# Performance work log

Hardware: AMD Instinct MI355X
Metric: run time of the kernel (lower is better)

Reference implementation:

```python
import jax, jax.numpy as jnp
import numpy as np

D_MODEL = 1024
N_HEADS = 16
D_K = D_MODEL // N_HEADS
THETA = 10000.0
B, S = 4, 2048


def _rope(x, positions):
    # x: [B, H, S, D_K]; positions: [S] int
    half = D_K // 2
    inv_freq = THETA ** (-jnp.arange(0, half, dtype=jnp.float32) * 2.0 / D_K)  # [half]
    ang = positions.astype(jnp.float32)[:, None] * inv_freq[None, :]  # [S, half]
    cos = jnp.cos(ang)[None, None, :, :]
    sin = jnp.sin(ang)[None, None, :, :]
    x_even = x[..., 0::2]
    x_odd = x[..., 1::2]
    out_even = x_even * cos - x_odd * sin
    out_odd = x_even * sin + x_odd * cos
    # interleave back to original layout
    out = jnp.stack([out_even, out_odd], axis=-1).reshape(x.shape)
    return out


def setup_inputs() -> dict:
    key = jax.random.key(0)
    ks = jax.random.split(key, 5)
    scale = 1.0 / np.sqrt(D_MODEL)
    return {
        "x": jax.random.normal(ks[0], (B, S, D_MODEL), dtype=jnp.float32),
        "token_positions": jnp.arange(S, dtype=jnp.int64 if jax.config.jax_enable_x64 else jnp.int32),
        "Wq": jax.random.normal(ks[1], (D_MODEL, D_MODEL), dtype=jnp.float32) * scale,
        "Wk": jax.random.normal(ks[2], (D_MODEL, D_MODEL), dtype=jnp.float32) * scale,
        "Wv": jax.random.normal(ks[3], (D_MODEL, D_MODEL), dtype=jnp.float32) * scale,
        "Wo": jax.random.normal(ks[4], (D_MODEL, D_MODEL), dtype=jnp.float32) * scale,
    }


def reference(x, token_positions, Wq, Wk, Wv, Wo):
    bsz, seq_len, _ = x.shape
    # projections (Linear_Transform: y = x @ W^T, no bias)
    def proj(W):
        h = jnp.einsum("bsd,ed->bse", x, W)
        return h.reshape(bsz, seq_len, N_HEADS, D_K).transpose(0, 2, 1, 3)  # [B,H,S,Dk]
    Q = proj(Wq)
    K = proj(Wk)
    V = proj(Wv)
    Q = _rope(Q, token_positions)
    K = _rope(K, token_positions)
    # scaled dot product attention with causal mask
    scores = jnp.einsum("bhqd,bhkd->bhqk", Q, K) / jnp.sqrt(jnp.float32(D_K))
    causal = jnp.tril(jnp.ones((seq_len, seq_len), dtype=bool))  # [S,S]
    scores = jnp.where(causal[None, None, :, :], scores, -jnp.inf)
    attn = jax.nn.softmax(scores, axis=-1)
    out = jnp.einsum("bhqk,bhkd->bhqd", attn, V)
    out = out.transpose(0, 2, 1, 3).reshape(bsz, seq_len, D_MODEL)
    return jnp.einsum("bsd,ed->bse", out, Wo)
```

## Files before the change

### kernel.cpp

```cpp
#include <hip/hip_runtime.h>
#include <hip/hip_bf16.h>
#include <cstdint>
#include <cstddef>

typedef __attribute__((ext_vector_type(4))) float f32x4;
typedef __attribute__((ext_vector_type(16))) float f32x16;
typedef __attribute__((ext_vector_type(8))) short bf16x8;
typedef unsigned int u32;
typedef unsigned short u16;


__device__ __forceinline__ u16 f2bf(float x) {
  u32 u = __builtin_bit_cast(u32, x);
  u += 0x7fffu + ((u >> 16) & 1u);
  return (u16)(u >> 16);
}

__device__ __forceinline__ u32 cvt_pk_bf16(float lo, float hi) {
  u32 r;
  asm("v_cvt_pk_bf16_f32 %0, %1, %2" : "=v"(r) : "v"(lo), "v"(hi));
  return r;
}

__device__ __forceinline__ void perm_swap(u32& a, u32& b) {
  asm("v_permlane32_swap_b32 %0, %1" : "+v"(a), "+v"(b));
}

__device__ __forceinline__ void gl_lds16(const void* g, void* l) {
  __builtin_amdgcn_global_load_lds(
      (const __attribute__((address_space(1))) u32*)(uintptr_t)g,
      (__attribute__((address_space(3))) u32*)(u32)(uintptr_t)l,
      16, 0, 0);
}

#define MFMA16(a, b, c) __builtin_amdgcn_mfma_f32_16x16x32_bf16((a), (b), (c), 0, 0, 0)
#define MFMA32(a, b, c) __builtin_amdgcn_mfma_f32_32x32x16_bf16((a), (b), (c), 0, 0, 0)


__global__ void cast_all_k(const float* __restrict__ x, const float* __restrict__ wq,
                           const float* __restrict__ wk, const float* __restrict__ wv,
                           const float* __restrict__ wo, u16* __restrict__ xb,
                           u16* __restrict__ wqb, u16* __restrict__ wkb,
                           u16* __restrict__ wvb, u16* __restrict__ wob) {
  int blk = blockIdx.x;
  const float* s; u16* d; int i;
  if (blk < 8192)       { s = x;  d = xb;  i = blk * 256; }
  else if (blk < 9216)  { s = wq; d = wqb; i = (blk - 8192) * 256; }
  else if (blk < 10240) { s = wk; d = wkb; i = (blk - 9216) * 256; }
  else if (blk < 11264) { s = wv; d = wvb; i = (blk - 10240) * 256; }
  else                  { s = wo; d = wob; i = (blk - 11264) * 256; }
  i += threadIdx.x;
  const float4 v = reinterpret_cast<const float4*>(s)[i];
  uint2 o;
  o.x = cvt_pk_bf16(v.x, v.y);
  o.y = cvt_pk_bf16(v.z, v.w);
  reinterpret_cast<uint2*>(d)[i] = o;
}


__global__ void rope_table_k(const int* __restrict__ pos, float2* __restrict__ cs) {
  int idx = blockIdx.x * 256 + threadIdx.x;
  int s = idx >> 5, i = idx & 31;
  float inv = powf(10000.0f, -(float)i * (1.0f / 32.0f));
  float ang = (float)pos[s] * inv;
  cs[idx] = float2{cosf(ang), sinf(ang)};
}


__global__ __launch_bounds__(256, 2)
void gemm_qkv(const u16* __restrict__ A, const u16* __restrict__ B,
              const float2* __restrict__ cs, u16* __restrict__ Qr,
              u16* __restrict__ Kr, u16* __restrict__ Vt, float qscale) {
  const int K = 1024;
  __shared__ u16 a_lds[2][128 * 32];
  __shared__ u16 b_lds[2][128 * 32];
  const int tid = threadIdx.x;
  const int l = tid & 63;
  const int w = tid >> 6;
  const int wm = w >> 1, wn = w & 1;
  const int bm = blockIdx.y, bn = blockIdx.x;

  const u16* Ab = A + (size_t)bm * 128 * K;
  const u16* Bb = B + (size_t)bn * 128 * K;

  auto stage = [&](int bq, int k0) {
#pragma unroll
    for (int half = 0; half < 2; ++half) {
      int t = half * 256 + tid;
      int row = t >> 2, slot = t & 3;
      int sp = slot ^ ((row >> 1) & 3);
      gl_lds16(Ab + (size_t)row * K + k0 + sp * 8, &a_lds[bq][t * 8]);
      gl_lds16(Bb + (size_t)row * K + k0 + sp * 8, &b_lds[bq][t * 8]);
    }
  };

  const f32x4 fz = {0.f, 0.f, 0.f, 0.f};
  f32x4 acc[4][4];
#pragma unroll
  for (int mi = 0; mi < 4; ++mi)
#pragma unroll
    for (int ni = 0; ni < 4; ++ni) acc[mi][ni] = fz;

  const int nk = K >> 5;
  stage(0, 0);
  int buf = 0;
  for (int kt = 0; kt < nk; ++kt) {
    __syncthreads();
    if (kt + 1 < nk) stage(buf ^ 1, (kt + 1) * 32);
    bf16x8 af[4], bf[4];
#pragma unroll
    for (int mi = 0; mi < 4; ++mi) {
      int row = wm * 64 + mi * 16 + (l & 15);
      int sp = (l >> 4) ^ ((row >> 1) & 3);
      af[mi] = *(const bf16x8*)&a_lds[buf][row * 32 + sp * 8];
    }
#pragma unroll
    for (int ni = 0; ni < 4; ++ni) {
      int row = wn * 64 + ni * 16 + (l & 15);
      int sp = (l >> 4) ^ ((row >> 1) & 3);
      bf[ni] = *(const bf16x8*)&b_lds[buf][row * 32 + sp * 8];
    }
#pragma unroll
    for (int mi = 0; mi < 4; ++mi)
#pragma unroll
      for (int ni = 0; ni < 4; ++ni)
        acc[mi][ni] = MFMA16(af[mi], bf[ni], acc[mi][ni]);
    buf ^= 1;
  }

  const int sector = bn >> 3;
  const int colb = ((bn & 7) << 7) + wn * 64;
  const int c = l & 15, h4 = l >> 4;

  if (sector == 2) {
#pragma unroll
    for (int mi = 0; mi < 4; ++mi) {
      int row = bm * 128 + wm * 64 + mi * 16 + 4 * h4;
      int b_ = row >> 11, s = row & 2047;
#pragma unroll
      for (int ni = 0; ni < 4; ++ni) {
        int cv = colb + ni * 16 + c;
        int hh = cv >> 6, dk = cv & 63;
        f32x4 v = acc[mi][ni];
        uint2 st;
        st.x = cvt_pk_bf16(v[0], v[1]);
        st.y = cvt_pk_bf16(v[2], v[3]);
        *(uint2*)&Vt[(((size_t)b_ * 16 + hh) << 17) + ((size_t)dk << 11) + s] = st;
      }
    }
  } else {
    u16* dst = sector ? Kr : Qr;
    const float scale = sector ? 1.0f : qscale;
#pragma unroll
    for (int mi = 0; mi < 4; ++mi) {
      int row0 = bm * 128 + wm * 64 + mi * 16 + 4 * h4;
#pragma unroll
      for (int ni = 0; ni < 4; ++ni) {
        int cv = colb + ni * 16 + c;
        int hh = cv >> 6, i2 = cv & 63;
        f32x4 v = acc[mi][ni];
        f32x4 pv;
#pragma unroll
        for (int j = 0; j < 4; ++j) pv[j] = __shfl_xor(v[j], 1);
        if (!(l & 1)) {
#pragma unroll
          for (int j = 0; j < 4; ++j) {
            int r = row0 + j, s = r & 2047, b_ = r >> 11;
            float2 t = cs[(s << 5) + (i2 >> 1)];
            float oe = (v[j] * t.x - pv[j] * t.y) * scale;
            float oo = (v[j] * t.y + pv[j] * t.x) * scale;
            *(u32*)&dst[(((size_t)(b_ * 16 + hh) * 2048 + s) << 6) + i2] =
                cvt_pk_bf16(oe, oo);
          }
        }
      }
    }
  }
}


__global__ __launch_bounds__(256, 2)
void gemm_bt(const u16* __restrict__ A, const u16* __restrict__ B,
             float* __restrict__ C, int M, int N, int K) {
  __shared__ u16 a_lds[2][128 * 32];
  __shared__ u16 b_lds[2][128 * 32];
  const int tid = threadIdx.x;
  const int l = tid & 63;
  const int w = tid >> 6;
  const int wm = w >> 1, wn = w & 1;
  const int bm = blockIdx.y, bn = blockIdx.x;

  const u16* Ab = A + (size_t)bm * 128 * K;
  const u16* Bb = B + (size_t)bn * 128 * K;

  auto stage = [&](int bq, int k0) {
#pragma unroll
    for (int half = 0; half < 2; ++half) {
      int t = half * 256 + tid;
      int row = t >> 2, slot = t & 3;
      int sp = slot ^ ((row >> 1) & 3);
      gl_lds16(Ab + (size_t)row * K + k0 + sp * 8, &a_lds[bq][t * 8]);
      gl_lds16(Bb + (size_t)row * K + k0 + sp * 8, &b_lds[bq][t * 8]);
    }
  };

  const f32x4 fz = {0.f, 0.f, 0.f, 0.f};
  f32x4 acc[4][4];
#pragma unroll
  for (int mi = 0; mi < 4; ++mi)
#pragma unroll
    for (int ni = 0; ni < 4; ++ni) acc[mi][ni] = fz;

  const int nk = K >> 5;
  stage(0, 0);
  int buf = 0;
  for (int kt = 0; kt < nk; ++kt) {
    __syncthreads();
    if (kt + 1 < nk) stage(buf ^ 1, (kt + 1) * 32);
    bf16x8 af[4], bf[4];
#pragma unroll
    for (int mi = 0; mi < 4; ++mi) {
      int row = wm * 64 + mi * 16 + (l & 15);
      int sp = (l >> 4) ^ ((row >> 1) & 3);
      af[mi] = *(const bf16x8*)&a_lds[buf][row * 32 + sp * 8];
    }
#pragma unroll
    for (int ni = 0; ni < 4; ++ni) {
      int row = wn * 64 + ni * 16 + (l & 15);
      int sp = (l >> 4) ^ ((row >> 1) & 3);
      bf[ni] = *(const bf16x8*)&b_lds[buf][row * 32 + sp * 8];
    }
#pragma unroll
    for (int mi = 0; mi < 4; ++mi)
#pragma unroll
      for (int ni = 0; ni < 4; ++ni)
        acc[mi][ni] = MFMA16(af[mi], bf[ni], acc[mi][ni]);
    buf ^= 1;
  }

#pragma unroll
  for (int mi = 0; mi < 4; ++mi) {
    int rbase = bm * 128 + wm * 64 + mi * 16 + ((l >> 4) << 2);
#pragma unroll
    for (int ni = 0; ni < 4; ++ni) {
      int col = bn * 128 + wn * 64 + ni * 16 + (l & 15);
      f32x4 v = acc[mi][ni];
#pragma unroll
      for (int j = 0; j < 4; ++j)
        C[(size_t)(rbase + j) * N + col] = v[j];
    }
  }
}


__global__ __launch_bounds__(256, 2)
void attn_k(const u16* __restrict__ Q, const u16* __restrict__ K,
            const u16* __restrict__ V, u16* __restrict__ O) {
  const int S = 2048;
  __shared__ u16 k_lds[2][64 * 64];
  __shared__ u16 v_lds[2][64 * 64];

  const int tid = threadIdx.x, l = tid & 63, w = tid >> 6;
  const int lane31 = l & 31, hi = l >> 5;

  const int wg = blockIdx.x;
  const int idx = (wg & 7) * 64 + (wg >> 3);
  const int bh = idx >> 3, pairI = idx & 7;

  const u16* Kb = K + (size_t)bh * S * 64;
  const u16* Vb = V + (size_t)bh * 64 * S;
  const int b = bh >> 4, hd = bh & 15;

  auto stageKV = [&](int bq, int kv0) {
#pragma unroll
    for (int half = 0; half < 2; ++half) {
      int t = half * 256 + tid;
      int row = t >> 3, slot = t & 7;
      int sp = slot ^ (row & 7);
      gl_lds16(Kb + (size_t)(kv0 + row) * 64 + sp * 8, &k_lds[bq][t * 8]);
      gl_lds16(Vb + (size_t)row * S + kv0 + sp * 8, &v_lds[bq][t * 8]);
    }
  };

#pragma unroll 1
  for (int ph = 0; ph < 2; ++ph) {
    const int qi = ph ? (15 - pairI) : pairI;
    const int q0 = qi * 128;
    const int nkv = 2 * qi + 2;
    const int qrow = q0 + w * 32 + lane31;
    const u16* Qp = Q + ((size_t)bh * S + qrow) * 64;

    bf16x8 qf[4];
#pragma unroll
    for (int ks = 0; ks < 4; ++ks)
      qf[ks] = *(const bf16x8*)(Qp + ks * 16 + hi * 8);
    __builtin_amdgcn_sched_barrier(0);
    stageKV(0, 0);

    f32x16 oacc[2];
#pragma unroll
    for (int dt = 0; dt < 2; ++dt)
#pragma unroll
      for (int r = 0; r < 16; ++r) oacc[dt][r] = 0.f;
    float m_run = -1e30f, l_run = 0.f;

    int buf = 0;
#pragma unroll 1
    for (int t = 0; t < nkv; ++t) {
      if (t + 1 < nkv) {
        stageKV(buf ^ 1, (t + 1) * 64);
        __builtin_amdgcn_sched_barrier(0);
        asm volatile("s_waitcnt vmcnt(4)" ::: "memory");
      } else {
        asm volatile("s_waitcnt vmcnt(0)" ::: "memory");
      }
      __builtin_amdgcn_sched_barrier(0);
      __builtin_amdgcn_s_barrier();
      __builtin_amdgcn_sched_barrier(0);

      f32x16 sc[2];
#pragma unroll
      for (int dt = 0; dt < 2; ++dt)
#pragma unroll
        for (int r = 0; r < 16; ++r) sc[dt][r] = 0.f;
      __builtin_amdgcn_s_setprio(1);
#pragma unroll
      for (int ks = 0; ks < 4; ++ks) {
        int sp = (2 * ks + hi) ^ (lane31 & 7);
#pragma unroll
        for (int dt = 0; dt < 2; ++dt) {
          bf16x8 kf = *(const bf16x8*)&k_lds[buf][(dt * 32 + lane31) * 64 + sp * 8];
          sc[dt] = MFMA32(kf, qf[ks], sc[dt]);
        }
      }
      __builtin_amdgcn_s_setprio(0);

      bf16x8 vf[2][4];
#pragma unroll
      for (int ks = 0; ks < 4; ++ks) {
        int sp = (2 * ks + hi) ^ (lane31 & 7);
#pragma unroll
        for (int dt = 0; dt < 2; ++dt)
          vf[dt][ks] = *(const bf16x8*)&v_lds[buf][(dt * 32 + lane31) * 64 + sp * 8];
      }

      if (t >= nkv - 2) {
#pragma unroll
        for (int dt = 0; dt < 2; ++dt)
#pragma unroll
          for (int r = 0; r < 16; ++r) {
            int kvg = t * 64 + dt * 32 + (r & 3) + 8 * (r >> 2) + 4 * hi;
            if (kvg > qrow) sc[dt][r] = -1e30f;
          }
      }

      float mx = -1e30f;
#pragma unroll
      for (int dt = 0; dt < 2; ++dt)
#pragma unroll
        for (int r = 0; r < 16; ++r) mx = fmaxf(mx, sc[dt][r]);
      mx = fmaxf(mx, __shfl_xor(mx, 32));

      const bool nores = __all(mx <= m_run);
      float mnew = nores ? m_run : fmaxf(m_run, mx);
      float ps = 0.f;
#pragma unroll
      for (int dt = 0; dt < 2; ++dt)
#pragma unroll
        for (int r = 0; r < 16; ++r) {
          float e = exp2f(sc[dt][r] - mnew);
          sc[dt][r] = e;
          ps += e;
        }
      ps += __shfl_xor(ps, 32);
      if (nores) {
        l_run += ps;
      } else {
        float alpha = exp2f(m_run - mnew);
        l_run = l_run * alpha + ps;
        m_run = mnew;
#pragma unroll
        for (int dt = 0; dt < 2; ++dt)
#pragma unroll
          for (int r = 0; r < 16; ++r) oacc[dt][r] *= alpha;
      }

      union { u32 u[4]; bf16x8 v; } pf[4];
#pragma unroll
      for (int ks = 0; ks < 4; ++ks) {
        const int sidx = ks >> 1, rb = (ks & 1) * 8;
        u32 c01 = cvt_pk_bf16(sc[sidx][rb + 0], sc[sidx][rb + 1]);
        u32 c23 = cvt_pk_bf16(sc[sidx][rb + 2], sc[sidx][rb + 3]);
        u32 c45 = cvt_pk_bf16(sc[sidx][rb + 4], sc[sidx][rb + 5]);
        u32 c67 = cvt_pk_bf16(sc[sidx][rb + 6], sc[sidx][rb + 7]);
        perm_swap(c01, c45);
        perm_swap(c23, c67);
        pf[ks].u[0] = c01; pf[ks].u[1] = c23; pf[ks].u[2] = c45; pf[ks].u[3] = c67;
      }

      __builtin_amdgcn_s_setprio(1);
#pragma unroll
      for (int dt = 0; dt < 2; ++dt)
#pragma unroll
        for (int ks = 0; ks < 4; ++ks)
          oacc[dt] = MFMA32(vf[dt][ks], pf[ks].v, oacc[dt]);
      __builtin_amdgcn_s_setprio(0);

      __builtin_amdgcn_sched_barrier(0);
      __builtin_amdgcn_s_barrier();
      __builtin_amdgcn_sched_barrier(0);
      buf ^= 1;
    }

    float inv = 1.f / l_run;
    u16* Ob = O + (((size_t)(b * 2048 + qrow)) << 10) + hd * 64;
#pragma unroll
    for (int dt = 0; dt < 2; ++dt)
#pragma unroll
      for (int g = 0; g < 4; ++g) {
        uint2 st;
        st.x = cvt_pk_bf16(oacc[dt][4 * g + 0] * inv, oacc[dt][4 * g + 1] * inv);
        st.y = cvt_pk_bf16(oacc[dt][4 * g + 2] * inv, oacc[dt][4 * g + 3] * inv);
        *(uint2*)&Ob[dt * 32 + g * 8 + hi * 4] = st;
      }
  }
}


extern "C" void kernel_launch(void* const* d_in, const int* in_sizes, int n_in,
                              void* d_out, int out_size, void* d_ws, size_t ws_size,
                              hipStream_t stream) {
  (void)in_sizes; (void)n_in; (void)out_size; (void)ws_size;
  const float* x  = (const float*)d_in[0];
  const int* pos  = (const int*)d_in[1];
  const float* Wq = (const float*)d_in[2];
  const float* Wk = (const float*)d_in[3];
  const float* Wv = (const float*)d_in[4];
  const float* Wo = (const float*)d_in[5];
  float* out = (float*)d_out;

  const int S = 2048, D = 1024;
  const size_t M = (size_t)4 * S;

  char* ws = (char*)d_ws;
  size_t off = 0;
  auto alloc = [&](size_t bytes) {
    void* p = ws + off;
    off += (bytes + 255) & ~(size_t)255;
    return p;
  };
  u16* xb   = (u16*)alloc(M * D * 2);
  u16* wqb  = (u16*)alloc((size_t)D * D * 2);
  u16* wkb  = (u16*)alloc((size_t)D * D * 2);
  u16* wvb  = (u16*)alloc((size_t)D * D * 2);
  u16* wob  = (u16*)alloc((size_t)D * D * 2);
  u16* Qr   = (u16*)alloc(M * D * 2);
  u16* Kr   = (u16*)alloc(M * D * 2);
  u16* Vt   = (u16*)alloc(M * D * 2);
  u16* Ob   = (u16*)alloc(M * D * 2);
  float2* csT = (float2*)alloc((size_t)S * 32 * 8);

  cast_all_k<<<12288, 256, 0, stream>>>(x, Wq, Wk, Wv, Wo, xb, wqb, wkb, wvb, wob);
  rope_table_k<<<(S * 32) / 256, 256, 0, stream>>>(pos, csT);

  const float QSCALE = 0.125f * 1.4426950408889634f;

  gemm_qkv<<<dim3(24, (unsigned)(M / 128)), 256, 0, stream>>>(
      xb, wqb, csT, Qr, Kr, Vt, QSCALE);
  attn_k<<<512, 256, 0, stream>>>(Qr, Kr, Vt, Ob);
  gemm_bt<<<dim3(8, (unsigned)(M / 128)), 256, 0, stream>>>(Ob, wob, out, (int)M, D, D);
}
```

Before: 197.1 us.

## Triple-buffer K/V staging in attention and use raw exp with tree reductions

The attention kernel moves from double to triple buffering of K/V tiles in LDS, prefetching two tiles ahead and dropping the end-of-iteration barrier, which removes one barrier per KV step. It also replaces exp2f with a raw v_exp_f32 inline asm and rewrites the row max and sum as tree reductions to shorten dependency chains. The larger LDS footprint may cut occupancy below the two blocks per CU requested by the launch bounds. With only one barrier per step, a buffer can still be read by slower waves when it is refilled, which risks a race.

```diff
diff --git a/kernel.cpp b/kernel.cpp
--- a/kernel.cpp
+++ b/kernel.cpp
@@ -19,6 +19,12 @@
 __device__ __forceinline__ u32 cvt_pk_bf16(float lo, float hi) {
   u32 r;
   asm("v_cvt_pk_bf16_f32 %0, %1, %2" : "=v"(r) : "v"(lo), "v"(hi));
+  return r;
+}
+
+__device__ __forceinline__ float fexp2(float x) {
+  float r;
+  asm("v_exp_f32 %0, %1\n\ts_nop 1" : "=v"(r) : "v"(x));
   return r;
 }
 
@@ -257,8 +263,8 @@
 void attn_k(const u16* __restrict__ Q, const u16* __restrict__ K,
             const u16* __restrict__ V, u16* __restrict__ O) {
   const int S = 2048;
-  __shared__ u16 k_lds[2][64 * 64];
-  __shared__ u16 v_lds[2][64 * 64];
+  __shared__ u16 k_lds[3][64 * 64];
+  __shared__ u16 v_lds[3][64 * 64];
 
   const int tid = threadIdx.x, l = tid & 63, w = tid >> 6;
   const int lane31 = l & 31, hi = l >> 5;
@@ -296,6 +302,7 @@
       qf[ks] = *(const bf16x8*)(Qp + ks * 16 + hi * 8);
     __builtin_amdgcn_sched_barrier(0);
     stageKV(0, 0);
+    stageKV(1, 64);
 
     f32x16 oacc[2];
 #pragma unroll
@@ -307,9 +314,12 @@
     int buf = 0;
 #pragma unroll 1
     for (int t = 0; t < nkv; ++t) {
-      if (t + 1 < nkv) {
-        stageKV(buf ^ 1, (t + 1) * 64);
+      if (t + 2 < nkv) {
+        int b2 = buf + 2; if (b2 >= 3) b2 -= 3;
+        stageKV(b2, (t + 2) * 64);
         __builtin_amdgcn_sched_barrier(0);
+        asm volatile("s_waitcnt vmcnt(8)" ::: "memory");
+      } else if (t + 1 < nkv) {
         asm volatile("s_waitcnt vmcnt(4)" ::: "memory");
       } else {
         asm volatile("s_waitcnt vmcnt(0)" ::: "memory");
@@ -354,29 +364,36 @@
           }
       }
 
-      float mx = -1e30f;
-#pragma unroll
-      for (int dt = 0; dt < 2; ++dt)
-#pragma unroll
-        for (int r = 0; r < 16; ++r) mx = fmaxf(mx, sc[dt][r]);
+      float r16[16];
+#pragma unroll
+      for (int i = 0; i < 16; ++i) r16[i] = fmaxf(sc[0][i], sc[1][i]);
+#pragma unroll
+      for (int i = 0; i < 8; ++i) r16[i] = fmaxf(r16[i], r16[i + 8]);
+#pragma unroll
+      for (int i = 0; i < 4; ++i) r16[i] = fmaxf(r16[i], r16[i + 4]);
+      float mx = fmaxf(fmaxf(r16[0], r16[1]), fmaxf(r16[2], r16[3]));
       mx = fmaxf(mx, __shfl_xor(mx, 32));
 
       const bool nores = __all(mx <= m_run);
       float mnew = nores ? m_run : fmaxf(m_run, mx);
-      float ps = 0.f;
 #pragma unroll
       for (int dt = 0; dt < 2; ++dt)
 #pragma unroll
-        for (int r = 0; r < 16; ++r) {
-          float e = exp2f(sc[dt][r] - mnew);
-          sc[dt][r] = e;
-          ps += e;
-        }
+        for (int r = 0; r < 16; ++r) sc[dt][r] = fexp2(sc[dt][r] - mnew);
+      float s16[16];
+#pragma unroll
+      for (int i = 0; i < 16; ++i) s16[i] = sc[0][i] + sc[1][i];
+#pragma unroll
+      for (int i = 0; i < 8; ++i) s16[i] += s16[i + 8];
+#pragma unroll
+      for (int i = 0; i < 4; ++i) s16[i] += s16[i + 4];
+      float ps = (s16[0] + s16[1]) + (s16[2] + s16[3]);
       ps += __shfl_xor(ps, 32);
+
       if (nores) {
         l_run += ps;
       } else {
-        float alpha = exp2f(m_run - mnew);
+        float alpha = fexp2(m_run - mnew);
         l_run = l_run * alpha + ps;
         m_run = mnew;
 #pragma unroll
@@ -406,11 +423,12 @@
           oacc[dt] = MFMA32(vf[dt][ks], pf[ks].v, oacc[dt]);
       __builtin_amdgcn_s_setprio(0);
 
-      __builtin_amdgcn_sched_barrier(0);
-      __builtin_amdgcn_s_barrier();
-      __builtin_amdgcn_sched_barrier(0);
-      buf ^= 1;
-    }
+      buf = (buf == 2) ? 0 : buf + 1;
+    }
+
+    __builtin_amdgcn_sched_barrier(0);
+    __builtin_amdgcn_s_barrier();
+    __builtin_amdgcn_sched_barrier(0);
 
     float inv = 1.f / l_run;
     u16* Ob = O + (((size_t)(b * 2048 + qrow)) << 10) + hd * 64;
```

Result: faster. 181.9 us (-7.7%).
